# Kernel tuning notes

Hardware: AMD Instinct MI355X
Metric: run time of the kernel (lower is better)

The kernel has to match this reference:

```python
import jax, jax.numpy as jnp
import numpy as np

N = 8192          # points per cloud
IN_C = 256        # in_channels
OUT_C = 256       # out_channels
SC = IN_C // 4    # shortcut_out_channels
KNN = 32          # neighbors gathered per point
KP = 15           # kernel points (standard KPConv)
RADIUS = 0.12
EXTENT = RADIUS * 2.0 / 2.5   # radius * kp_extent / conv_radius
NEG_SLOPE = 0.1
EPS = 1e-5


def setup_inputs() -> dict:
    key = jax.random.key(0)
    ks = jax.random.split(key, 10)
    src = jax.random.normal(ks[0], (N, IN_C), jnp.float32)
    tgt = jax.random.normal(ks[1], (N, IN_C), jnp.float32)
    src_coords = jax.random.uniform(ks[2], (N, 3), jnp.float32)
    tgt_coords = jax.random.uniform(ks[3], (N, 3), jnp.float32)
    W_in = jax.random.normal(ks[4], (IN_C, SC), jnp.float32) / np.sqrt(IN_C)
    b_in = jnp.zeros((SC,), jnp.float32)
    kernel_pts = jax.random.normal(ks[5], (KP, 3), jnp.float32) * (0.7 * EXTENT)
    W_kp = jax.random.normal(ks[6], (KP, SC, SC), jnp.float32) / np.sqrt(KP * SC)
    W_out = jax.random.normal(ks[7], (SC, OUT_C), jnp.float32) / np.sqrt(SC)
    b_out = jnp.zeros((OUT_C,), jnp.float32)
    gamma = jnp.ones((OUT_C,), jnp.float32)
    beta = jnp.zeros((OUT_C,), jnp.float32)
    return dict(src=src, tgt=tgt, src_coords=src_coords, tgt_coords=tgt_coords,
                W_in=W_in, b_in=b_in, kernel_pts=kernel_pts, W_kp=W_kp,
                W_out=W_out, b_out=b_out, gamma=gamma, beta=beta)


def _one_cloud(x, coords, W_in, b_in, kernel_pts, W_kp, W_out, b_out, gamma, beta):
    # 1x1 conv in: [N, IN_C] -> [N, SC]
    h = x @ W_in + b_in

    # neighbor search: kNN by squared distance, masked to the conv radius
    d2 = jnp.sum((coords[:, None, :] - coords[None, :, :]) ** 2, axis=-1)  # [N, N]
    _, idx = jax.lax.top_k(-d2, KNN)                                       # [N, KNN]
    nb_coords = coords[idx]                                                # [N, KNN, 3]
    rel = nb_coords - coords[:, None, :]                                   # [N, KNN, 3]
    in_range = jnp.sum(rel ** 2, axis=-1) <= RADIUS ** 2                   # [N, KNN]

    # KPConv: linear correlation to kernel points, masked neighbor aggregate
    diff = rel[:, :, None, :] - kernel_pts[None, None, :, :]               # [N, KNN, KP, 3]
    dist = jnp.sqrt(jnp.sum(diff ** 2, axis=-1))                           # [N, KNN, KP]
    infl = jnp.maximum(1.0 - dist / EXTENT, 0.0) * in_range[:, :, None]    # [N, KNN, KP]
    nb_feats = h[idx]                                                      # [N, KNN, SC]
    agg = jnp.einsum('nkp,nkc->npc', infl, nb_feats)                       # [N, KP, SC]
    h = jnp.einsum('npc,pcd->nd', agg, W_kp)                               # [N, SC]

    # 1x1 conv out: [N, SC] -> [N, OUT_C]
    y = h @ W_out + b_out

    # batch norm over points (training-mode statistics) + affine
    mu = jnp.mean(y, axis=0)
    var = jnp.mean((y - mu) ** 2, axis=0)
    y = gamma * (y - mu) * jax.lax.rsqrt(var + EPS) + beta

    # leaky relu
    return jnp.where(y > 0, y, NEG_SLOPE * y)


def reference(src, tgt, src_coords, tgt_coords, W_in, b_in, kernel_pts, W_kp,
              W_out, b_out, gamma, beta):
    params = (W_in, b_in, kernel_pts, W_kp, W_out, b_out, gamma, beta)
    s = _one_cloud(src, src_coords, *params)
    t = _one_cloud(tgt, tgt_coords, *params)
    return (s, t, src_coords, tgt_coords)
```

## Files before the change

kernel.cpp:

```cpp
#include <hip/hip_runtime.h>
#include <stdint.h>

#define NPTS 8192
#define KNN 32
#define KPN 15
#define SCC 64
#define OUTC 256
#define R2F 0.0144f
#define INV_EXT (1.0f/0.096f)
#define SCAP 128
#define NT 8
#define COB 32
#define GD 8
#define NCELL (GD*GD*GD)
#define KJ (KPN*SCC)
#define AGP 968

typedef float  f32x4  __attribute__((ext_vector_type(4)));
typedef __bf16 bf16x8 __attribute__((ext_vector_type(8)));

__device__ __forceinline__ int cell_of(float x) {
  int c = (int)(x * (float)GD);
  return c < 0 ? 0 : (c > GD-1 ? GD-1 : c);
}

__global__ __launch_bounds__(256) void win_cvt(
    const float* __restrict__ W, __bf16* __restrict__ WinF)
{
  int i = blockIdx.x*256 + threadIdx.x;
  int j = i & 7, lane = (i >> 3) & 63, cc = i >> 9;
  int kc = cc >> 2, ct = cc & 3;
  int g16 = lane >> 4, p = lane & 15;
  int k = kc*32 + g16*8 + j;
  WinF[i] = (__bf16)W[(size_t)k*64 + ct*16 + p];
}

__global__ __launch_bounds__(128) void conv_in_mfma(
    const float* __restrict__ src, const float* __restrict__ tgt,
    const __bf16* __restrict__ WinF, const float* __restrict__ b,
    __bf16* __restrict__ h)
{
  int t = threadIdx.x;
  int w = t >> 6, lane = t & 63;
  int rt = blockIdx.x*2 + w;
  int row0 = rt*16;
  const float* x = (row0 >> 13) ? tgt : src;
  int n0 = row0 & 8191;
  int g16 = lane >> 4, p = lane & 15;
  const float* xrow = x + (size_t)(n0 + p)*256;
  f32x4 acc[4];
  #pragma unroll
  for (int ct = 0; ct < 4; ++ct) {
    float bb = b[ct*16 + p];
    acc[ct] = (f32x4){bb, bb, bb, bb};
  }
  #pragma unroll
  for (int kc = 0; kc < 8; ++kc) {
    float4 xa = *(const float4*)(xrow + kc*32 + g16*8);
    float4 xb = *(const float4*)(xrow + kc*32 + g16*8 + 4);
    bf16x8 af;
    af[0]=(__bf16)xa.x; af[1]=(__bf16)xa.y; af[2]=(__bf16)xa.z; af[3]=(__bf16)xa.w;
    af[4]=(__bf16)xb.x; af[5]=(__bf16)xb.y; af[6]=(__bf16)xb.z; af[7]=(__bf16)xb.w;
    #pragma unroll
    for (int ct = 0; ct < 4; ++ct) {
      bf16x8 bf = *(const bf16x8*)(WinF + (size_t)(kc*4 + ct)*512 + lane*8);
      acc[ct] = __builtin_amdgcn_mfma_f32_16x16x32_bf16(af, bf, acc[ct], 0,0,0);
    }
  }
  #pragma unroll
  for (int ct = 0; ct < 4; ++ct)
    #pragma unroll
    for (int r = 0; r < 4; ++r)
      h[(size_t)(row0 + g16*4 + r)*SCC + ct*16 + p] = (__bf16)acc[ct][r];
}

__global__ __launch_bounds__(256) void grid_count(
    const float* __restrict__ cA, const float* __restrict__ cB,
    unsigned int* __restrict__ hist)
{
  int i = blockIdx.x*256 + threadIdx.x;
  int cloud = i >> 13, n = i & 8191;
  const float* coords = cloud ? cB : cA;
  int cx = cell_of(coords[(size_t)n*3]);
  int cy = cell_of(coords[(size_t)n*3+1]);
  int cz = cell_of(coords[(size_t)n*3+2]);
  atomicAdd(&hist[cloud*NCELL + (cz*GD + cy)*GD + cx], 1u);
}

__global__ __launch_bounds__(512) void grid_scan(
    const unsigned int* __restrict__ hist,
    unsigned int* __restrict__ starts,
    unsigned int* __restrict__ cursor)
{
  __shared__ unsigned int a[NCELL], b[NCELL];
  int t = threadIdx.x;
  for (int cloud = 0; cloud < 2; ++cloud) {
    unsigned int v = hist[cloud*NCELL + t];
    a[t] = v; __syncthreads();
    unsigned int *src = a, *dst = b;
    for (int off = 1; off < NCELL; off <<= 1) {
      unsigned int x = src[t];
      if (t >= off) x += src[t - off];
      dst[t] = x; __syncthreads();
      unsigned int* tmp = src; src = dst; dst = tmp;
    }
    unsigned int inc = src[t];
    unsigned int exc = inc - v;
    starts[cloud*520 + t] = exc;
    cursor[cloud*NCELL + t] = exc;
    if (t == NCELL-1) starts[cloud*520 + NCELL] = inc;
    __syncthreads();
  }
}

__global__ __launch_bounds__(256) void grid_scatter(
    const float* __restrict__ cA, const float* __restrict__ cB,
    unsigned int* __restrict__ cursor, float4* __restrict__ sorted)
{
  int i = blockIdx.x*256 + threadIdx.x;
  int cloud = i >> 13, n = i & 8191;
  const float* coords = cloud ? cB : cA;
  float x = coords[(size_t)n*3], y = coords[(size_t)n*3+1], z = coords[(size_t)n*3+2];
  int cell = (cell_of(z)*GD + cell_of(y))*GD + cell_of(x);
  unsigned int slot = atomicAdd(&cursor[cloud*NCELL + cell], 1u);
  sorted[(size_t)cloud*NPTS + slot] = make_float4(x, y, z, __int_as_float(n));
}

__global__ __launch_bounds__(256) void knn_grid(
    const float* __restrict__ cA, const float* __restrict__ cB,
    const unsigned int* __restrict__ starts, const float4* __restrict__ sorted,
    short* __restrict__ fidx)
{
  __shared__ unsigned long long surv[4][SCAP];
  int t = threadIdx.x, w = t >> 6, lane = t & 63;
  int q = blockIdx.x*4 + w;
  int cloud = q >> 13, n = q & 8191;
  const float* coords = cloud ? cB : cA;
  float qx = coords[(size_t)n*3];
  float qy = coords[(size_t)n*3+1];
  float qz = coords[(size_t)n*3+2];
  int cx = cell_of(qx), cy = cell_of(qy), cz = cell_of(qz);
  const unsigned int* st = starts + cloud*520;
  const float4* sp = sorted + (size_t)cloud*NPTS;
  int c0 = cx > 0 ? cx-1 : 0;
  int c1 = cx < GD-1 ? cx+1 : GD-1;
  unsigned int cnt = 0;
  for (int dz = -1; dz <= 1; ++dz) {
    int zz = cz + dz; if (zz < 0 || zz > GD-1) continue;
    for (int dy = -1; dy <= 1; ++dy) {
      int yy = cy + dy; if (yy < 0 || yy > GD-1) continue;
      int rb = (zz*GD + yy)*GD;
      unsigned int s = st[rb + c0];
      unsigned int e = st[rb + c1 + 1];
      for (unsigned int jj = s; jj < e; jj += 64) {
        unsigned int j = jj + lane;
        bool keep = false; float d2 = 0.f; unsigned int oi = 0;
        if (j < e) {
          float4 p = sp[j];
          float dx = qx-p.x, dyy = qy-p.y, dzz = qz-p.z;
          d2 = fmaf(dx, dx, fmaf(dyy, dyy, dzz*dzz));
          oi = __float_as_uint(p.w);
          keep = (d2 <= R2F);
        }
        unsigned long long m = __ballot(keep);
        if (keep) {
          unsigned int before = __builtin_amdgcn_mbcnt_hi(
              (unsigned int)(m >> 32),
              __builtin_amdgcn_mbcnt_lo((unsigned int)m, 0u));
          unsigned int pos = cnt + before;
          if (pos < SCAP)
            surv[w][pos] = ((unsigned long long)__float_as_uint(d2) << 32) | oi;
        }
        cnt += (unsigned int)__popcll(m);
      }
    }
  }
  int C = (int)cnt; if (C > SCAP) C = SCAP;
  unsigned long long k0 = (lane      < C) ? surv[w][lane]      : ~0ULL;
  unsigned long long k1 = (lane + 64 < C) ? surv[w][lane + 64] : ~0ULL;
  int r0 = 0, r1 = 0;
  for (int j = 0; j < C; ++j) {
    unsigned long long kj = surv[w][j];
    r0 += (kj < k0);
    r1 += (kj < k1);
  }
  size_t g = (size_t)cloud*NPTS + n;
  if (k0 != ~0ULL && r0 < KNN) fidx[g*KNN + r0] = (short)(k0 & 0xffffu);
  if (k1 != ~0ULL && r1 < KNN) fidx[g*KNN + r1] = (short)(k1 & 0xffffu);
  if (lane >= C && lane < KNN) fidx[g*KNN + lane] = (short)-1;
}

__global__ __launch_bounds__(512) void kpconv_fused(
    const float* __restrict__ cA, const float* __restrict__ cB,
    const float* __restrict__ kpts, const short* __restrict__ fidx,
    const __bf16* __restrict__ h, const __bf16* __restrict__ WkpT,
    float* __restrict__ h2)
{
  __shared__ __bf16 agg_s[NT][AGP];
  __shared__ float  red2[2*4*16*17];
  int t = threadIdx.x;
  int w = t >> 6, lane = t & 63;
  int gq = blockIdx.x*NT + w;
  int cloud = gq >> 13, n = gq & 8191;
  const float* coords = cloud ? cB : cA;
  int idxreg = fidx[(size_t)gq*KNN + (lane & 31)];
  float qx = coords[(size_t)n*3];
  float qy = coords[(size_t)n*3+1];
  float qz = coords[(size_t)n*3+2];
  int g16 = lane >> 4;
  int p   = lane & 15;
  int pc  = p < KPN ? p : 0;
  float kpx = kpts[pc*3], kpy = kpts[pc*3+1], kpz = kpts[pc*3+2];
  bf16x8 afrag;
  int idxs[8];
  #pragma unroll
  for (int j = 0; j < 8; ++j) {
    int k = g16*8 + j;
    int idx = __shfl(idxreg, k);
    idxs[j] = idx < 0 ? 0 : idx;
    float wv = 0.f;
    if (idx >= 0 && p < KPN) {
      float rx = coords[(size_t)idx*3]   - qx;
      float ry = coords[(size_t)idx*3+1] - qy;
      float rz = coords[(size_t)idx*3+2] - qz;
      float dx = rx - kpx, dy = ry - kpy, dz = rz - kpz;
      float d = sqrtf(fmaf(dx, dx, fmaf(dy, dy, dz*dz)));
      wv = fmaxf(1.0f - d*INV_EXT, 0.0f);
    }
    afrag[j] = (__bf16)wv;
  }
  bf16x8 bfrag0, bfrag1, bfrag2, bfrag3;
  #pragma unroll
  for (int j = 0; j < 8; ++j) {
    const __bf16* hrow = h + ((size_t)(cloud*NPTS + idxs[j]))*SCC + p;
    bfrag0[j] = hrow[0];
    bfrag1[j] = hrow[16];
    bfrag2[j] = hrow[32];
    bfrag3[j] = hrow[48];
  }
  f32x4 acc0 = {0.f,0.f,0.f,0.f}, acc1 = acc0, acc2 = acc0, acc3 = acc0;
  acc0 = __builtin_amdgcn_mfma_f32_16x16x32_bf16(afrag, bfrag0, acc0, 0, 0, 0);
  acc1 = __builtin_amdgcn_mfma_f32_16x16x32_bf16(afrag, bfrag1, acc1, 0, 0, 0);
  acc2 = __builtin_amdgcn_mfma_f32_16x16x32_bf16(afrag, bfrag2, acc2, 0, 0, 0);
  acc3 = __builtin_amdgcn_mfma_f32_16x16x32_bf16(afrag, bfrag3, acc3, 0, 0, 0);
  #pragma unroll
  for (int r = 0; r < 4; ++r) {
    int pp = g16*4 + r;
    if (pp < KPN) {
      agg_s[w][pp*SCC +      p] = (__bf16)acc0[r];
      agg_s[w][pp*SCC + 16 + p] = (__bf16)acc1[r];
      agg_s[w][pp*SCC + 32 + p] = (__bf16)acc2[r];
      agg_s[w][pp*SCC + 48 + p] = (__bf16)acc3[r];
    }
  }
  __syncthreads();
  {
    int dt = w & 3, kh = w >> 2;
    int ptb = p & 7;
    const __bf16* arow = WkpT + (size_t)(dt*16 + p)*KJ + kh*480 + g16*8;
    const __bf16* brow = &agg_s[ptb][kh*480 + g16*8];
    f32x4 accB = {0.f,0.f,0.f,0.f};
    #pragma unroll
    for (int s = 0; s < 15; ++s) {
      bf16x8 af = *(const bf16x8*)(arow + s*32);
      bf16x8 bf = *(const bf16x8*)(brow + s*32);
      accB = __builtin_amdgcn_mfma_f32_16x16x32_bf16(af, bf, accB, 0, 0, 0);
    }
    if (p < 8) {
      #pragma unroll
      for (int r = 0; r < 4; ++r)
        red2[((kh*4 + dt)*16 + g16*4 + r)*17 + p] = accB[r];
    }
  }
  __syncthreads();
  {
    int pt = t >> 6, d = t & 63;
    float v = red2[d*17 + pt] + red2[(64 + d)*17 + pt];
    h2[((size_t)blockIdx.x*NT + pt)*SCC + d] = v;
  }
}

__global__ __launch_bounds__(512) void conv_out_bn(
    const float* __restrict__ h2, const float* __restrict__ W,
    const float* __restrict__ b, float* __restrict__ y,
    float* __restrict__ stats)
{
  __shared__ float w_s[SCC*OUTC];
  __shared__ float h_s[COB][SCC];
  __shared__ float rs_s[2][OUTC];
  __shared__ float rs2_s[2][OUTC];
  int t = threadIdx.x;
  int d = t & 255, rg = t >> 8;
  int row0 = blockIdx.x*COB;
  int cloud = (int)(blockIdx.x >> 8);
  {
    const float4* gw = (const float4*)W;
    float4* lw = (float4*)w_s;
    #pragma unroll
    for (int i = 0; i < 8; ++i) lw[t + 512*i] = gw[t + 512*i];
    const float4* gh = (const float4*)(h2 + (size_t)row0*SCC);
    ((float4*)h_s)[t] = gh[t];
  }
  __syncthreads();
  float acc[16];
  float bb = b[d];
  #pragma unroll
  for (int r = 0; r < 16; ++r) acc[r] = bb;
  int rb = rg*16;
  #pragma unroll 4
  for (int c4 = 0; c4 < 16; ++c4) {
    float w0 = w_s[(c4*4+0)*OUTC + d];
    float w1 = w_s[(c4*4+1)*OUTC + d];
    float w2 = w_s[(c4*4+2)*OUTC + d];
    float w3 = w_s[(c4*4+3)*OUTC + d];
    #pragma unroll
    for (int r = 0; r < 16; ++r) {
      float4 hv = *(const float4*)&h_s[rb + r][c4*4];
      acc[r] = fmaf(hv.x,w0, fmaf(hv.y,w1, fmaf(hv.z,w2, fmaf(hv.w,w3, acc[r]))));
    }
  }
  float s = 0.f, s2 = 0.f;
  #pragma unroll
  for (int r = 0; r < 16; ++r) {
    float v = acc[r];
    y[((size_t)row0 + rb + r)*OUTC + d] = v;
    s += v; s2 = fmaf(v, v, s2);
  }
  rs_s[rg][d] = s; rs2_s[rg][d] = s2;
  __syncthreads();
  if (rg == 0) {
    atomicAdd(&stats[cloud*512 + d],       s  + rs_s[1][d]);
    atomicAdd(&stats[cloud*512 + 256 + d], s2 + rs2_s[1][d]);
  }
}

__global__ __launch_bounds__(256) void bn_apply_k(
    float* __restrict__ y, const float* __restrict__ stats,
    const float* __restrict__ gamma, const float* __restrict__ beta)
{
  size_t e = (size_t)blockIdx.x*256 + threadIdx.x;
  int c = (int)(e & 255);
  int cloud = (int)(e >> 21);
  float s  = stats[cloud*512 + c];
  float s2 = stats[cloud*512 + 256 + c];
  float mu  = s * (1.0f/NPTS);
  float var = fmaxf(s2 * (1.0f/NPTS) - mu*mu, 0.f);
  float sc = gamma[c] * rsqrtf(var + 1e-5f);
  float sh = beta[c] - mu*sc;
  float v = fmaf(y[e], sc, sh);
  v = v > 0.f ? v : 0.1f*v;
  y[e] = v;
}

__global__ __launch_bounds__(256) void wkp_cvt(
    const float* __restrict__ Wkp, __bf16* __restrict__ WkpT)
{
  int i = blockIdx.x*256 + threadIdx.x;
  int j = i >> 6, d = i & 63;
  WkpT[(size_t)d*KJ + j] = (__bf16)Wkp[i];
}

__global__ __launch_bounds__(256) void emit_coords(
    const float* __restrict__ scd, const float* __restrict__ tcd,
    float* __restrict__ out, float* __restrict__ stats,
    unsigned int* __restrict__ hist)
{
  int b = blockIdx.x;
  int t = threadIdx.x;
  if (b == 192) {
    for (int i = t; i < 1024; i += 256) { stats[i] = 0.f; hist[i] = 0u; }
    return;
  }
  int i = b*256 + t;
  out[i] = (i < NPTS*3) ? scd[i] : tcd[i - NPTS*3];
}

extern "C" void kernel_launch(void* const* d_in, const int* in_sizes, int n_in,
                              void* d_out, int out_size, void* d_ws, size_t ws_size,
                              hipStream_t stream)
{
  (void)in_sizes; (void)n_in; (void)out_size; (void)ws_size;
  const float* src   = (const float*)d_in[0];
  const float* tgt   = (const float*)d_in[1];
  const float* scd   = (const float*)d_in[2];
  const float* tcd   = (const float*)d_in[3];
  const float* W_in  = (const float*)d_in[4];
  const float* b_in  = (const float*)d_in[5];
  const float* kpts  = (const float*)d_in[6];
  const float* W_kp  = (const float*)d_in[7];
  const float* W_out = (const float*)d_in[8];
  const float* b_out = (const float*)d_in[9];
  const float* gamma = (const float*)d_in[10];
  const float* beta  = (const float*)d_in[11];

  char* ws = (char*)d_ws;
  __bf16* h    = (__bf16*)ws;
  float* h2    = (float*)(ws + (4u<<20));
  short* fidx  = (short*)(ws + (8u<<20));
  float* stats = (float*)(ws + (9u<<20));
  __bf16* WkpT = (__bf16*)(ws + (9u<<20) + (64u<<10));
  __bf16* WinF = (__bf16*)(ws + (9u<<20) + (256u<<10));
  unsigned int* hist   = (unsigned int*)(ws + (4u<<20));
  unsigned int* starts = (unsigned int*)(ws + (4u<<20) + (8u<<10));
  unsigned int* cursor = (unsigned int*)(ws + (4u<<20) + (16u<<10));
  float4* sorted       = (float4*)(ws + (4u<<20) + (32u<<10));

  float* yout = (float*)d_out;

  emit_coords<<<193, 256, 0, stream>>>(scd, tcd, yout + (size_t)2*NPTS*OUTC,
                                       stats, hist);
  wkp_cvt<<<240, 256, 0, stream>>>(W_kp, WkpT);
  win_cvt<<<64, 256, 0, stream>>>(W_in, WinF);
  grid_count<<<64, 256, 0, stream>>>(scd, tcd, hist);
  grid_scan<<<1, 512, 0, stream>>>(hist, starts, cursor);
  grid_scatter<<<64, 256, 0, stream>>>(scd, tcd, cursor, sorted);
  knn_grid<<<4096, 256, 0, stream>>>(scd, tcd, starts, sorted, fidx);
  conv_in_mfma<<<512, 128, 0, stream>>>(src, tgt, WinF, b_in, h);
  kpconv_fused<<<2048, 512, 0, stream>>>(scd, tcd, kpts, fidx, h, WkpT, h2);
  conv_out_bn<<<512, 512, 0, stream>>>(h2, W_out, b_out, yout, stats);
  bn_apply_k<<<16384, 256, 0, stream>>>(yout, stats, gamma, beta);
}
```

Baseline: 198.0 us.

## Merge small launches, fuse grid count/scan, co-schedule conv_in with kNN

Collapses coordinate copy and weight conversions into one prep kernel, and merges histogram counting (now in shared memory), stats zeroing and scan into a single 1024-thread block. It also appends the conv_in MFMA blocks to the kNN launch so both run concurrently, which cuts the launch count from 11 to 7. Separately, kpconv_fused now preloads its WkpT fragments into registers before the barrier and sets a min-blocks occupancy hint. The single-block grid build serialises 16K points through one CU, and the register preload may raise register pressure.

```diff
diff --git a/kernel.cpp b/kernel.cpp
--- a/kernel.cpp
+++ b/kernel.cpp
@@ -24,91 +24,71 @@
   return c < 0 ? 0 : (c > GD-1 ? GD-1 : c);
 }
 
-__global__ __launch_bounds__(256) void win_cvt(
-    const float* __restrict__ W, __bf16* __restrict__ WinF)
-{
-  int i = blockIdx.x*256 + threadIdx.x;
-  int j = i & 7, lane = (i >> 3) & 63, cc = i >> 9;
-  int kc = cc >> 2, ct = cc & 3;
-  int g16 = lane >> 4, p = lane & 15;
-  int k = kc*32 + g16*8 + j;
-  WinF[i] = (__bf16)W[(size_t)k*64 + ct*16 + p];
-}
-
-__global__ __launch_bounds__(128) void conv_in_mfma(
-    const float* __restrict__ src, const float* __restrict__ tgt,
-    const __bf16* __restrict__ WinF, const float* __restrict__ b,
-    __bf16* __restrict__ h)
-{
-  int t = threadIdx.x;
-  int w = t >> 6, lane = t & 63;
-  int rt = blockIdx.x*2 + w;
-  int row0 = rt*16;
-  const float* x = (row0 >> 13) ? tgt : src;
-  int n0 = row0 & 8191;
-  int g16 = lane >> 4, p = lane & 15;
-  const float* xrow = x + (size_t)(n0 + p)*256;
-  f32x4 acc[4];
-  #pragma unroll
-  for (int ct = 0; ct < 4; ++ct) {
-    float bb = b[ct*16 + p];
-    acc[ct] = (f32x4){bb, bb, bb, bb};
-  }
-  #pragma unroll
-  for (int kc = 0; kc < 8; ++kc) {
-    float4 xa = *(const float4*)(xrow + kc*32 + g16*8);
-    float4 xb = *(const float4*)(xrow + kc*32 + g16*8 + 4);
-    bf16x8 af;
-    af[0]=(__bf16)xa.x; af[1]=(__bf16)xa.y; af[2]=(__bf16)xa.z; af[3]=(__bf16)xa.w;
-    af[4]=(__bf16)xb.x; af[5]=(__bf16)xb.y; af[6]=(__bf16)xb.z; af[7]=(__bf16)xb.w;
-    #pragma unroll
-    for (int ct = 0; ct < 4; ++ct) {
-      bf16x8 bf = *(const bf16x8*)(WinF + (size_t)(kc*4 + ct)*512 + lane*8);
-      acc[ct] = __builtin_amdgcn_mfma_f32_16x16x32_bf16(af, bf, acc[ct], 0,0,0);
-    }
-  }
-  #pragma unroll
-  for (int ct = 0; ct < 4; ++ct)
-    #pragma unroll
-    for (int r = 0; r < 4; ++r)
-      h[(size_t)(row0 + g16*4 + r)*SCC + ct*16 + p] = (__bf16)acc[ct][r];
-}
-
-__global__ __launch_bounds__(256) void grid_count(
+__global__ __launch_bounds__(256) void prep_k(
+    const float* __restrict__ scd, const float* __restrict__ tcd,
+    float* __restrict__ out,
+    const float* __restrict__ Wkp, __bf16* __restrict__ WkpT,
+    const float* __restrict__ Win, __bf16* __restrict__ WinF)
+{
+  int b = blockIdx.x, t = threadIdx.x;
+  if (b < 192) {
+    int i = b*256 + t;
+    out[i] = (i < NPTS*3) ? scd[i] : tcd[i - NPTS*3];
+  } else if (b < 432) {
+    int i = (b - 192)*256 + t;
+    int j = i >> 6, d = i & 63;
+    WkpT[(size_t)d*KJ + j] = (__bf16)Wkp[i];
+  } else {
+    int i = (b - 432)*256 + t;
+    int j = i & 7, lane = (i >> 3) & 63, cc = i >> 9;
+    int kc = cc >> 2, ct = cc & 3;
+    int g16 = lane >> 4, p = lane & 15;
+    int k = kc*32 + g16*8 + j;
+    WinF[i] = (__bf16)Win[(size_t)k*64 + ct*16 + p];
+  }
+}
+
+__global__ __launch_bounds__(1024) void grid_build(
     const float* __restrict__ cA, const float* __restrict__ cB,
-    unsigned int* __restrict__ hist)
-{
-  int i = blockIdx.x*256 + threadIdx.x;
-  int cloud = i >> 13, n = i & 8191;
-  const float* coords = cloud ? cB : cA;
-  int cx = cell_of(coords[(size_t)n*3]);
-  int cy = cell_of(coords[(size_t)n*3+1]);
-  int cz = cell_of(coords[(size_t)n*3+2]);
-  atomicAdd(&hist[cloud*NCELL + (cz*GD + cy)*GD + cx], 1u);
-}
-
-__global__ __launch_bounds__(512) void grid_scan(
-    const unsigned int* __restrict__ hist,
     unsigned int* __restrict__ starts,
-    unsigned int* __restrict__ cursor)
-{
+    unsigned int* __restrict__ cursor,
+    float* __restrict__ stats)
+{
+  __shared__ unsigned int hcnt[2][NCELL];
   __shared__ unsigned int a[NCELL], b[NCELL];
   int t = threadIdx.x;
+  if (t < NCELL) { hcnt[0][t] = 0u; hcnt[1][t] = 0u; }
+  stats[t] = 0.f;
+  __syncthreads();
+  for (int i = t; i < 2*NPTS; i += 1024) {
+    int cloud = i >> 13, n = i & 8191;
+    const float* coords = cloud ? cB : cA;
+    int cx = cell_of(coords[(size_t)n*3]);
+    int cy = cell_of(coords[(size_t)n*3+1]);
+    int cz = cell_of(coords[(size_t)n*3+2]);
+    atomicAdd(&hcnt[cloud][(cz*GD + cy)*GD + cx], 1u);
+  }
+  __syncthreads();
   for (int cloud = 0; cloud < 2; ++cloud) {
-    unsigned int v = hist[cloud*NCELL + t];
-    a[t] = v; __syncthreads();
-    unsigned int *src = a, *dst = b;
+    if (t < NCELL) a[t] = hcnt[cloud][t];
+    __syncthreads();
+    unsigned int *s = a, *d = b;
     for (int off = 1; off < NCELL; off <<= 1) {
-      unsigned int x = src[t];
-      if (t >= off) x += src[t - off];
-      dst[t] = x; __syncthreads();
-      unsigned int* tmp = src; src = dst; dst = tmp;
-    }
-    unsigned int inc = src[t];
-    unsigned int exc = inc - v;
-    starts[cloud*520 + t] = exc;
-    cursor[cloud*NCELL + t] = exc;
-    if (t == NCELL-1) starts[cloud*520 + NCELL] = inc;
+      if (t < NCELL) {
+        unsigned int x = s[t];
+        if (t >= off) x += s[t - off];
+        d[t] = x;
+      }
+      __syncthreads();
+      unsigned int* tmp = s; s = d; d = tmp;
+    }
+    if (t < NCELL) {
+      unsigned int inc = s[t];
+      unsigned int exc = inc - hcnt[cloud][t];
+      starts[cloud*520 + t] = exc;
+      cursor[cloud*NCELL + t] = exc;
+      if (t == NCELL-1) starts[cloud*520 + NCELL] = inc;
+    }
     __syncthreads();
   }
 }
@@ -126,14 +106,51 @@
   sorted[(size_t)cloud*NPTS + slot] = make_float4(x, y, z, __int_as_float(n));
 }
 
-__global__ __launch_bounds__(256) void knn_grid(
+__global__ __launch_bounds__(256) void knn_convin_k(
     const float* __restrict__ cA, const float* __restrict__ cB,
     const unsigned int* __restrict__ starts, const float4* __restrict__ sorted,
-    short* __restrict__ fidx)
+    short* __restrict__ fidx,
+    const float* __restrict__ src, const float* __restrict__ tgt,
+    const __bf16* __restrict__ WinF, const float* __restrict__ bin,
+    __bf16* __restrict__ h)
 {
   __shared__ unsigned long long surv[4][SCAP];
+  int bId = blockIdx.x;
   int t = threadIdx.x, w = t >> 6, lane = t & 63;
-  int q = blockIdx.x*4 + w;
+  if (bId >= 4096) {
+    int rt = (bId - 4096)*4 + w;
+    int row0 = rt*16;
+    const float* x = (row0 >> 13) ? tgt : src;
+    int n0 = row0 & 8191;
+    int g16 = lane >> 4, p = lane & 15;
+    const float* xrow = x + (size_t)(n0 + p)*256;
+    f32x4 acc[4];
+    #pragma unroll
+    for (int ct = 0; ct < 4; ++ct) {
+      float bb = bin[ct*16 + p];
+      acc[ct] = (f32x4){bb, bb, bb, bb};
+    }
+    #pragma unroll
+    for (int kc = 0; kc < 8; ++kc) {
+      float4 xa = *(const float4*)(xrow + kc*32 + g16*8);
+      float4 xb = *(const float4*)(xrow + kc*32 + g16*8 + 4);
+      bf16x8 af;
+      af[0]=(__bf16)xa.x; af[1]=(__bf16)xa.y; af[2]=(__bf16)xa.z; af[3]=(__bf16)xa.w;
+      af[4]=(__bf16)xb.x; af[5]=(__bf16)xb.y; af[6]=(__bf16)xb.z; af[7]=(__bf16)xb.w;
+      #pragma unroll
+      for (int ct = 0; ct < 4; ++ct) {
+        bf16x8 bf = *(const bf16x8*)(WinF + (size_t)(kc*4 + ct)*512 + lane*8);
+        acc[ct] = __builtin_amdgcn_mfma_f32_16x16x32_bf16(af, bf, acc[ct], 0,0,0);
+      }
+    }
+    #pragma unroll
+    for (int ct = 0; ct < 4; ++ct)
+      #pragma unroll
+      for (int r = 0; r < 4; ++r)
+        h[(size_t)(row0 + g16*4 + r)*SCC + ct*16 + p] = (__bf16)acc[ct][r];
+    return;
+  }
+  int q = bId*4 + w;
   int cloud = q >> 13, n = q & 8191;
   const float* coords = cloud ? cB : cA;
   float qx = coords[(size_t)n*3];
@@ -156,10 +173,10 @@
         unsigned int j = jj + lane;
         bool keep = false; float d2 = 0.f; unsigned int oi = 0;
         if (j < e) {
-          float4 p = sp[j];
-          float dx = qx-p.x, dyy = qy-p.y, dzz = qz-p.z;
+          float4 p4 = sp[j];
+          float dx = qx-p4.x, dyy = qy-p4.y, dzz = qz-p4.z;
           d2 = fmaf(dx, dx, fmaf(dyy, dyy, dzz*dzz));
-          oi = __float_as_uint(p.w);
+          oi = __float_as_uint(p4.w);
           keep = (d2 <= R2F);
         }
         unsigned long long m = __ballot(keep);
@@ -190,7 +207,7 @@
   if (lane >= C && lane < KNN) fidx[g*KNN + lane] = (short)-1;
 }
 
-__global__ __launch_bounds__(512) void kpconv_fused(
+__global__ __launch_bounds__(512, 4) void kpconv_fused(
     const float* __restrict__ cA, const float* __restrict__ cB,
     const float* __restrict__ kpts, const short* __restrict__ fidx,
     const __bf16* __restrict__ h, const __bf16* __restrict__ WkpT,
@@ -253,18 +270,20 @@
       agg_s[w][pp*SCC + 48 + p] = (__bf16)acc3[r];
     }
   }
+  int dt = w & 3, kh = w >> 2;
+  const __bf16* arow = WkpT + (size_t)(dt*16 + p)*KJ + kh*480 + g16*8;
+  bf16x8 afB[15];
+  #pragma unroll
+  for (int s = 0; s < 15; ++s) afB[s] = *(const bf16x8*)(arow + s*32);
   __syncthreads();
   {
-    int dt = w & 3, kh = w >> 2;
     int ptb = p & 7;
-    const __bf16* arow = WkpT + (size_t)(dt*16 + p)*KJ + kh*480 + g16*8;
     const __bf16* brow = &agg_s[ptb][kh*480 + g16*8];
     f32x4 accB = {0.f,0.f,0.f,0.f};
     #pragma unroll
     for (int s = 0; s < 15; ++s) {
-      bf16x8 af = *(const bf16x8*)(arow + s*32);
-      bf16x8 bf = *(const bf16x8*)(brow + s*32);
-      accB = __builtin_amdgcn_mfma_f32_16x16x32_bf16(af, bf, accB, 0, 0, 0);
+      bf16x8 bfr = *(const bf16x8*)(brow + s*32);
+      accB = __builtin_amdgcn_mfma_f32_16x16x32_bf16(afB[s], bfr, accB, 0, 0, 0);
     }
     if (p < 8) {
       #pragma unroll
@@ -350,29 +369,6 @@
   float v = fmaf(y[e], sc, sh);
   v = v > 0.f ? v : 0.1f*v;
   y[e] = v;
-}
-
-__global__ __launch_bounds__(256) void wkp_cvt(
-    const float* __restrict__ Wkp, __bf16* __restrict__ WkpT)
-{
-  int i = blockIdx.x*256 + threadIdx.x;
-  int j = i >> 6, d = i & 63;
-  WkpT[(size_t)d*KJ + j] = (__bf16)Wkp[i];
-}
-
-__global__ __launch_bounds__(256) void emit_coords(
-    const float* __restrict__ scd, const float* __restrict__ tcd,
-    float* __restrict__ out, float* __restrict__ stats,
-    unsigned int* __restrict__ hist)
-{
-  int b = blockIdx.x;
-  int t = threadIdx.x;
-  if (b == 192) {
-    for (int i = t; i < 1024; i += 256) { stats[i] = 0.f; hist[i] = 0u; }
-    return;
-  }
-  int i = b*256 + t;
-  out[i] = (i < NPTS*3) ? scd[i] : tcd[i - NPTS*3];
 }
 
 extern "C" void kernel_launch(void* const* d_in, const int* in_sizes, int n_in,
@@ -400,22 +396,18 @@
   float* stats = (float*)(ws + (9u<<20));
   __bf16* WkpT = (__bf16*)(ws + (9u<<20) + (64u<<10));
   __bf16* WinF = (__bf16*)(ws + (9u<<20) + (256u<<10));
-  unsigned int* hist   = (unsigned int*)(ws + (4u<<20));
   unsigned int* starts = (unsigned int*)(ws + (4u<<20) + (8u<<10));
   unsigned int* cursor = (unsigned int*)(ws + (4u<<20) + (16u<<10));
   float4* sorted       = (float4*)(ws + (4u<<20) + (32u<<10));
 
   float* yout = (float*)d_out;
 
-  emit_coords<<<193, 256, 0, stream>>>(scd, tcd, yout + (size_t)2*NPTS*OUTC,
-                                       stats, hist);
-  wkp_cvt<<<240, 256, 0, stream>>>(W_kp, WkpT);
-  win_cvt<<<64, 256, 0, stream>>>(W_in, WinF);
-  grid_count<<<64, 256, 0, stream>>>(scd, tcd, hist);
-  grid_scan<<<1, 512, 0, stream>>>(hist, starts, cursor);
+  prep_k<<<496, 256, 0, stream>>>(scd, tcd, yout + (size_t)2*NPTS*OUTC,
+                                  W_kp, WkpT, W_in, WinF);
+  grid_build<<<1, 1024, 0, stream>>>(scd, tcd, starts, cursor, stats);
   grid_scatter<<<64, 256, 0, stream>>>(scd, tcd, cursor, sorted);
-  knn_grid<<<4096, 256, 0, stream>>>(scd, tcd, starts, sorted, fidx);
-  conv_in_mfma<<<512, 128, 0, stream>>>(src, tgt, WinF, b_in, h);
+  knn_convin_k<<<4352, 256, 0, stream>>>(scd, tcd, starts, sorted, fidx,
+                                         src, tgt, WinF, b_in, h);
   kpconv_fused<<<2048, 512, 0, stream>>>(scd, tcd, kpts, fidx, h, WkpT, h2);
   conv_out_bn<<<512, 512, 0, stream>>>(h2, W_out, b_out, yout, stats);
   bn_apply_k<<<16384, 256, 0, stream>>>(yout, stats, gamma, beta);
```

Measured after the change: 204.0 us. 3.0% more time.
